# Kernel optimization log

Hardware: AMD Instinct MI355X
Metric: run time of the kernel (lower is better)

The kernel has to match this reference:

```python
import jax, jax.numpy as jnp
import numpy as np

B, S, D, H = 4, 1024, 1024, 16
DK = D // H
NEG = -1e9


def setup_inputs() -> dict:
    key = jax.random.key(0)
    ks = jax.random.split(key, 14)
    sc = 1.0 / np.sqrt(D)
    inp = {
        "query": jax.random.normal(ks[0], (B, S, D), jnp.float32),
        "key": jax.random.normal(ks[1], (B, S, D), jnp.float32),
        "value": jax.random.normal(ks[2], (B, S, D), jnp.float32),
        "mask": jax.random.randint(ks[3], (B, S, S), 0, 2, jnp.int32),
        "group_prob": jax.random.uniform(ks[4], (B, S, S), jnp.float32),
        "Wq": jax.random.normal(ks[5], (D, D), jnp.float32) * sc,
        "bq": jnp.zeros((D,), jnp.float32),
        "Wk": jax.random.normal(ks[6], (D, D), jnp.float32) * sc,
        "bk": jnp.zeros((D,), jnp.float32),
        "Wv": jax.random.normal(ks[7], (D, D), jnp.float32) * sc,
        "bv": jnp.zeros((D,), jnp.float32),
        "Wo": jax.random.normal(ks[8], (D, D), jnp.float32) * sc,
        "bo": jnp.zeros((D,), jnp.float32),
    }
    return inp


def reference(query, key, value, mask, group_prob, Wq, bq, Wk, bk, Wv, bv, Wo, bo):
    # QKV projections, split heads: [B,S,D] -> [B,H,S,DK]
    def proj(x, W, b):
        return (x @ W.T + b).reshape(B, S, H, DK).transpose(0, 2, 1, 3)

    q = proj(query, Wq, bq)
    k = proj(key, Wk, bk)
    v = proj(value, Wv, bv)

    scores = jnp.einsum("bhqd,bhkd->bhqk", q, k) / jnp.sqrt(jnp.float32(DK))

    # group_prob branch: allowed where mask OR diagonal is nonzero
    diag = jnp.eye(S, dtype=jnp.int32)
    allowed = (mask[:, None, :, :] | diag[None, None, :, :]) != 0  # [B,1,S,S]
    scores = jnp.where(allowed, scores, NEG)

    p_attn = jax.nn.softmax(scores, axis=-1)
    p_attn = p_attn * group_prob[:, None, :, :]  # post-softmax group reweighting

    x = jnp.einsum("bhqk,bhkd->bhqd", p_attn, v)
    x = x.transpose(0, 2, 1, 3).reshape(B, S, D)
    return x @ Wo.T + bo
```

## Files before the change

kernel.cpp:

```cpp
#include <hip/hip_runtime.h>
#include <hip/hip_bf16.h>


#define AS1q __attribute__((address_space(1)))
#define AS3q __attribute__((address_space(3)))

typedef __attribute__((ext_vector_type(8))) __bf16 bf16x8;
typedef __attribute__((ext_vector_type(4))) float f32x4;
typedef __attribute__((ext_vector_type(8))) unsigned short u16x8;

#define GSTR 40

__device__ __forceinline__ void gload_lds16(const void* g, void* l) {
  __builtin_amdgcn_global_load_lds((const AS1q void*)g, (AS3q void*)l, 16, 0, 0);
}
__device__ __forceinline__ bf16x8 lds_read8(const unsigned short* p) {
  bf16x8 r;
  __builtin_memcpy(&r, __builtin_assume_aligned(p, 16), 16);
  return r;
}
__device__ __forceinline__ void lds_write8(unsigned short* p, const void* v) {
  __builtin_memcpy(__builtin_assume_aligned(p, 16), v, 16);
}
__device__ __forceinline__ u16x8 cvt8h(const float4 a, const float4 b) {
  const float fv[8] = {a.x, a.y, a.z, a.w, b.x, b.y, b.z, b.w};
  union { u16x8 v; __bf16 e[8]; } hh;
#pragma unroll
  for (int i = 0; i < 8; ++i) hh.e[i] = (__bf16)fv[i];
  return hh.v;
}
__device__ __forceinline__ void cvt8hl(const float4 a, const float4 b, u16x8* hi, u16x8* lo) {
  const float fv[8] = {a.x, a.y, a.z, a.w, b.x, b.y, b.z, b.w};
  union { u16x8 v; __bf16 e[8]; } hh, ll;
#pragma unroll
  for (int i = 0; i < 8; ++i) {
    const __bf16 h = (__bf16)fv[i];
    hh.e[i] = h;
    ll.e[i] = (__bf16)(fv[i] - (float)h);
  }
  *hi = hh.v; *lo = ll.v;
}
__device__ __forceinline__ unsigned short bfbits(float f) {
  const __bf16 h = (__bf16)f;
  unsigned short u; __builtin_memcpy(&u, &h, 2); return u;
}

__global__ __launch_bounds__(256) void k_prep_g2(
    const int* __restrict__ Mask, const float* __restrict__ Gp, float* __restrict__ G2)
{
  const size_t f = (size_t)blockIdx.x * 256 + threadIdx.x;
  const size_t e = f << 2;
  const int k0 = (int)(e & 1023), q = (int)((e >> 10) & 1023);
  const int4 m4 = *(const int4*)(Mask + e);
  const float4 g4 = *(const float4*)(Gp + e);
  float4 r;
  r.x = (m4.x | (q == k0 + 0)) ? g4.x : -1.f;
  r.y = (m4.y | (q == k0 + 1)) ? g4.y : -1.f;
  r.z = (m4.z | (q == k0 + 2)) ? g4.z : -1.f;
  r.w = (m4.w | (q == k0 + 3)) ? g4.w : -1.f;
  *(float4*)(G2 + e) = r;
}

__global__ __launch_bounds__(256) void k_prep_w(
    const float* __restrict__ Wq, const float* __restrict__ Wk,
    const float* __restrict__ Wv,
    unsigned short* __restrict__ Qw, unsigned short* __restrict__ Kw,
    unsigned short* __restrict__ Vw)
{
  const int z = blockIdx.z;
  const size_t e = ((size_t)blockIdx.x * 256 + threadIdx.x) * 8;
  const float* S = (z == 0) ? Wq : (z == 1) ? Wk : Wv;
  unsigned short* D = (z == 0) ? Qw : (z == 1) ? Kw : Vw;
  const float4 a = *(const float4*)(S + e);
  const float4 b = *(const float4*)(S + e + 4);
  *(u16x8*)(D + e) = cvt8h(a, b);
}

__global__ __launch_bounds__(256) void k_gemm_qkv(
    const float* __restrict__ X0, const float* __restrict__ X1, const float* __restrict__ X2,
    const unsigned short* __restrict__ W0, const unsigned short* __restrict__ W1,
    const unsigned short* __restrict__ W2,
    const float* __restrict__ B0, const float* __restrict__ B1, const float* __restrict__ B2,
    unsigned short* __restrict__ O0, unsigned short* __restrict__ O1,
    unsigned short* __restrict__ O2)
{
  const int z = blockIdx.z;
  const float* X = (z == 0) ? X0 : (z == 1) ? X1 : X2;
  const unsigned short* W = (z == 0) ? W0 : (z == 1) ? W1 : W2;
  const float* Bi = (z == 0) ? B0 : (z == 1) ? B1 : B2;
  unsigned short* O = (z == 0) ? O0 : (z == 1) ? O1 : O2;

  const int bid = blockIdx.x;
  const int swz = (bid & 7) * 64 + (bid >> 3);
  const int n0 = (swz & 15) * 64, m0 = (swz >> 4) * 128;

  __shared__ alignas(16) unsigned short Ah[2][128 * GSTR];
  __shared__ alignas(16) unsigned short Bh[2][64 * GSTR];
  const int tid = threadIdx.x, l = tid & 63, w = tid >> 6;
  const int wr = w >> 1, wc = w & 1;

  f32x4 acc[4][2];
#pragma unroll
  for (int i = 0; i < 4; ++i)
#pragma unroll
    for (int j = 0; j < 2; ++j) acc[i][j] = (f32x4){0.f, 0.f, 0.f, 0.f};

  const int arow = tid >> 1, ac0 = (tid & 1) * 16;
  const int brow = tid >> 2, bc0 = (tid & 3) * 8;
  const float* xsrc = X + (size_t)(m0 + arow) * 1024 + ac0;
  const unsigned short* wsrc = W + (size_t)(n0 + brow) * 1024 + bc0;

  float4 fx[4];
  u16x8 bx;
#pragma unroll
  for (int i = 0; i < 4; ++i) fx[i] = *(const float4*)(xsrc + i * 4);
  bx = *(const u16x8*)(wsrc);
  {
    const u16x8 a0 = cvt8h(fx[0], fx[1]), a1 = cvt8h(fx[2], fx[3]);
    lds_write8(&Ah[0][arow * GSTR + ac0], &a0);
    lds_write8(&Ah[0][arow * GSTR + ac0 + 8], &a1);
    lds_write8(&Bh[0][brow * GSTR + bc0], &bx);
  }
#pragma unroll
  for (int i = 0; i < 4; ++i) fx[i] = *(const float4*)(xsrc + 32 + i * 4);
  bx = *(const u16x8*)(wsrc + 32);

  int buf = 0;
  for (int kt = 0; kt < 32; ++kt) {
    __syncthreads();
    if (kt < 31) {
      const u16x8 a0 = cvt8h(fx[0], fx[1]), a1 = cvt8h(fx[2], fx[3]);
      lds_write8(&Ah[buf ^ 1][arow * GSTR + ac0], &a0);
      lds_write8(&Ah[buf ^ 1][arow * GSTR + ac0 + 8], &a1);
      lds_write8(&Bh[buf ^ 1][brow * GSTR + bc0], &bx);
      if (kt < 30) {
        const float* nx = xsrc + (kt + 2) * 32;
#pragma unroll
        for (int i = 0; i < 4; ++i) fx[i] = *(const float4*)(nx + i * 4);
        bx = *(const u16x8*)(wsrc + (kt + 2) * 32);
      }
    }
    bf16x8 ah[4], bh[2];
#pragma unroll
    for (int mf = 0; mf < 4; ++mf) {
      const int r = wr * 64 + mf * 16 + (l & 15);
      ah[mf] = lds_read8(&Ah[buf][r * GSTR + (l >> 4) * 8]);
    }
#pragma unroll
    for (int nf = 0; nf < 2; ++nf) {
      const int r = wc * 32 + nf * 16 + (l & 15);
      bh[nf] = lds_read8(&Bh[buf][r * GSTR + (l >> 4) * 8]);
    }
#pragma unroll
    for (int mf = 0; mf < 4; ++mf)
#pragma unroll
      for (int nf = 0; nf < 2; ++nf)
        acc[mf][nf] = __builtin_amdgcn_mfma_f32_16x16x32_bf16(ah[mf], bh[nf], acc[mf][nf], 0, 0, 0);
    buf ^= 1;
  }

#pragma unroll
  for (int nf = 0; nf < 2; ++nf) {
    const int col = n0 + wc * 32 + nf * 16 + (l & 15);
    const float bias = Bi[col];
#pragma unroll
    for (int mf = 0; mf < 4; ++mf) {
      const int rbase = m0 + wr * 64 + mf * 16 + (l >> 4) * 4;
#pragma unroll
      for (int j = 0; j < 4; ++j)
        O[(size_t)(rbase + j) * 1024 + col] = bfbits(acc[mf][nf][j] + bias);
    }
  }
}

__global__ __launch_bounds__(256) void k_gemm_out(
    const unsigned short* __restrict__ X, const float* __restrict__ W,
    const float* __restrict__ Bi, float* __restrict__ Out)
{
  const int bid = blockIdx.x;
  const int swz = (bid & 7) * 128 + (bid >> 3);
  const int n0 = (swz & 15) * 64, m0 = (swz >> 4) * 64;

  __shared__ alignas(16) unsigned short Ah[64 * GSTR];
  __shared__ alignas(16) unsigned short Bh[64 * GSTR], Bl[64 * GSTR];
  const int tid = threadIdx.x, l = tid & 63, w = tid >> 6;
  const int wr = w >> 1, wc = w & 1;

  f32x4 acc[2][2];
#pragma unroll
  for (int i = 0; i < 2; ++i)
#pragma unroll
    for (int j = 0; j < 2; ++j) acc[i][j] = (f32x4){0.f, 0.f, 0.f, 0.f};

  const int srow = tid >> 2, sc0 = (tid & 3) * 8;
  const unsigned short* xsrc = X + (size_t)(m0 + srow) * 1024 + sc0;
  const float* wsrc = W + (size_t)(n0 + srow) * 1024 + sc0;

  u16x8 xcur = *(const u16x8*)xsrc;
  float4 fw[2];
#pragma unroll
  for (int i = 0; i < 2; ++i) fw[i] = *(const float4*)(wsrc + i * 4);

  for (int kt = 0; kt < 32; ++kt) {
    const u16x8 xstage = xcur;
    u16x8 wh1, wl1;
    cvt8hl(fw[0], fw[1], &wh1, &wl1);
    if (kt < 31) {
      xcur = *(const u16x8*)(xsrc + (kt + 1) * 32);
      const float* nw = wsrc + (kt + 1) * 32;
#pragma unroll
      for (int i = 0; i < 2; ++i) fw[i] = *(const float4*)(nw + i * 4);
    }
    __syncthreads();
    lds_write8(&Ah[srow * GSTR + sc0], &xstage);
    lds_write8(&Bh[srow * GSTR + sc0], &wh1);
    lds_write8(&Bl[srow * GSTR + sc0], &wl1);
    __syncthreads();

    bf16x8 ah[2], bh[2], bl[2];
#pragma unroll
    for (int mf = 0; mf < 2; ++mf) {
      const int r = wr * 32 + mf * 16 + (l & 15);
      ah[mf] = lds_read8(&Ah[r * GSTR + (l >> 4) * 8]);
    }
#pragma unroll
    for (int nf = 0; nf < 2; ++nf) {
      const int r = wc * 32 + nf * 16 + (l & 15);
      bh[nf] = lds_read8(&Bh[r * GSTR + (l >> 4) * 8]);
      bl[nf] = lds_read8(&Bl[r * GSTR + (l >> 4) * 8]);
    }
#pragma unroll
    for (int mf = 0; mf < 2; ++mf)
#pragma unroll
      for (int nf = 0; nf < 2; ++nf) {
        acc[mf][nf] = __builtin_amdgcn_mfma_f32_16x16x32_bf16(ah[mf], bh[nf], acc[mf][nf], 0, 0, 0);
        acc[mf][nf] = __builtin_amdgcn_mfma_f32_16x16x32_bf16(ah[mf], bl[nf], acc[mf][nf], 0, 0, 0);
      }
  }

#pragma unroll
  for (int nf = 0; nf < 2; ++nf) {
    const int col = n0 + wc * 32 + nf * 16 + (l & 15);
    const float bias = Bi[col];
#pragma unroll
    for (int mf = 0; mf < 2; ++mf) {
      const int rbase = m0 + wr * 32 + mf * 16 + (l >> 4) * 4;
#pragma unroll
      for (int j = 0; j < 4; ++j)
        Out[(size_t)(rbase + j) * 1024 + col] = acc[mf][nf][j] + bias;
    }
  }
}

__global__ __launch_bounds__(256) void k_attn(
    const unsigned short* Qh, const unsigned short* __restrict__ Kb,
    const unsigned short* __restrict__ Vb,
    const float* __restrict__ G2, unsigned short* Xo)
{
  const int i = blockIdx.x;
  const int xc = i & 7, kk_ = i >> 3;
  const int h = kk_ & 15, g = kk_ >> 4;
  const int qb = g * 8 + xc;
  const int qt = qb >> 2, b = qb & 3;

  __shared__ alignas(16) unsigned short Kh[2][64 * 64];
  __shared__ alignas(16) unsigned short Vh[64 * 64];
  __shared__ alignas(16) unsigned short Ph[64 * 64];
  const int tid = threadIdx.x, l = tid & 63, w = tid >> 6;

  const unsigned short* kb_ = Kb + (size_t)b * 1048576 + h * 64;
  const unsigned short* vb_ = Vb + (size_t)b * 1048576 + h * 64;

  bf16x8 aq[2];
  {
    const int qrow = qt * 64 + w * 16 + (l & 15);
    const unsigned short* qp_ = Qh + ((size_t)(b * 1024 + qrow)) * 1024 + h * 64;
    aq[0] = lds_read8(qp_ + (l >> 4) * 8);
    aq[1] = lds_read8(qp_ + 32 + (l >> 4) * 8);
  }

  f32x4 accO[4];
#pragma unroll
  for (int nf = 0; nf < 4; ++nf) accO[nf] = (f32x4){0.f, 0.f, 0.f, 0.f};
  float zacc[4] = {0.f, 0.f, 0.f, 0.f};

  const int qloc0 = w * 16 + (l >> 4) * 4;
  const int qg0 = qt * 64 + qloc0;
  const int mcol = l & 15;

  const float* grow[4];
#pragma unroll
  for (int j = 0; j < 4; ++j)
    grow[j] = G2 + (((size_t)(b * 1024 + qg0 + j)) << 10) + mcol;

  const int srcg8 = ((l & 7) ^ (l >> 3)) * 8;
  const int rowl = l >> 3;
  const int kb4 = (tid & 15) * 4, db4 = (tid >> 4) * 4;
  union U4 { unsigned int u[2]; unsigned short s[4]; };
  U4 vr[4];

#pragma unroll
  for (int I = 0; I < 2; ++I)
    gload_lds16(kb_ + (size_t)(I * 32 + w * 8 + rowl) * 1024 + srcg8,
                &Kh[0][I * 2048 + w * 512]);
#pragma unroll
  for (int ii = 0; ii < 4; ++ii)
    __builtin_memcpy(&vr[ii], vb_ + (size_t)(kb4 + ii) * 1024 + db4, 8);

  float gcur[4][4], gnext[4][4];
#pragma unroll
  for (int nf = 0; nf < 4; ++nf)
#pragma unroll
    for (int j = 0; j < 4; ++j) gcur[nf][j] = grow[j][nf * 16];

  int buf = 0;
  for (int kt = 0; kt < 16; ++kt) {
    __syncthreads();

#pragma unroll
    for (int ii = 0; ii < 4; ++ii) {
      const int d = db4 + ii;
      union { unsigned short s[4]; unsigned long long v; } pk;
#pragma unroll
      for (int u = 0; u < 4; ++u) pk.s[u] = vr[u].s[ii];
      const int c = kb4 ^ ((d & 7) << 3);
      __builtin_memcpy(__builtin_assume_aligned(&Vh[d * 64 + c], 8), &pk.v, 8);
    }
    __syncthreads();

    if (kt < 15) {
#pragma unroll
      for (int I = 0; I < 2; ++I)
        gload_lds16(kb_ + (size_t)((kt + 1) * 64 + I * 32 + w * 8 + rowl) * 1024 + srcg8,
                    &Kh[buf ^ 1][I * 2048 + w * 512]);
#pragma unroll
      for (int ii = 0; ii < 4; ++ii)
        __builtin_memcpy(&vr[ii], vb_ + (size_t)((kt + 1) * 64 + kb4 + ii) * 1024 + db4, 8);
#pragma unroll
      for (int nf = 0; nf < 4; ++nf)
#pragma unroll
        for (int j = 0; j < 4; ++j) gnext[nf][j] = grow[j][(kt + 1) * 64 + nf * 16];
    }

#pragma unroll
    for (int nf = 0; nf < 4; ++nf) {
      f32x4 sacc = (f32x4){0.f, 0.f, 0.f, 0.f};
      const int kr = nf * 16 + (l & 15);
#pragma unroll
      for (int ks = 0; ks < 2; ++ks) {
        const int c = (ks * 32 + (l >> 4) * 8) ^ ((kr & 7) << 3);
        sacc = __builtin_amdgcn_mfma_f32_16x16x32_bf16(aq[ks], lds_read8(&Kh[buf][kr * 64 + c]), sacc, 0, 0, 0);
      }
#pragma unroll
      for (int j = 0; j < 4; ++j) {
        const float g2 = gcur[nf][j];
        const float e = (g2 >= 0.f) ? exp2f(fmaf(sacc[j], 0.18033688f, -17.31234049f)) : 0.f;
        zacc[j] += e;
        const int qloc = qloc0 + j;
        Ph[qloc * 64 + ((nf * 16 + mcol) ^ ((qloc & 7) << 3))] = bfbits(e * g2);
      }
    }
    bf16x8 pah[2];
    {
      const int ar = w * 16 + (l & 15);
#pragma unroll
      for (int ks = 0; ks < 2; ++ks) {
        const int c = (ks * 32 + (l >> 4) * 8) ^ ((ar & 7) << 3);
        pah[ks] = lds_read8(&Ph[ar * 64 + c]);
      }
    }
#pragma unroll
    for (int nf = 0; nf < 4; ++nf) {
      const int dr = nf * 16 + (l & 15);
#pragma unroll
      for (int ks = 0; ks < 2; ++ks) {
        const int c = (ks * 32 + (l >> 4) * 8) ^ ((dr & 7) << 3);
        accO[nf] = __builtin_amdgcn_mfma_f32_16x16x32_bf16(pah[ks], lds_read8(&Vh[dr * 64 + c]), accO[nf], 0, 0, 0);
      }
    }
    buf ^= 1;
#pragma unroll
    for (int nf = 0; nf < 4; ++nf)
#pragma unroll
      for (int j = 0; j < 4; ++j) gcur[nf][j] = gnext[nf][j];
  }

#pragma unroll
  for (int j = 0; j < 4; ++j) {
#pragma unroll
    for (int off = 1; off < 16; off <<= 1) zacc[j] += __shfl_xor(zacc[j], off, 64);
  }
  float rz[4];
#pragma unroll
  for (int j = 0; j < 4; ++j) rz[j] = 1.f / zacc[j];

#pragma unroll
  for (int nf = 0; nf < 4; ++nf) {
    const int d = nf * 16 + (l & 15);
#pragma unroll
    for (int j = 0; j < 4; ++j) {
      const int qg = qg0 + j;
      Xo[((size_t)(b * 1024 + qg)) * 1024 + h * 64 + d] = bfbits(accO[nf][j] * rz[j]);
    }
  }
}

extern "C" void kernel_launch(void* const* d_in, const int* in_sizes, int n_in,
                              void* d_out, int out_size, void* d_ws, size_t ws_size,
                              hipStream_t stream) {
  const float* query = (const float*)d_in[0];
  const float* key_in = (const float*)d_in[1];
  const float* value = (const float*)d_in[2];
  const int* mask = (const int*)d_in[3];
  const float* gp = (const float*)d_in[4];
  const float* Wq = (const float*)d_in[5];
  const float* bq = (const float*)d_in[6];
  const float* Wk = (const float*)d_in[7];
  const float* bk = (const float*)d_in[8];
  const float* Wv = (const float*)d_in[9];
  const float* bv = (const float*)d_in[10];
  const float* Wo = (const float*)d_in[11];
  const float* bo = (const float*)d_in[12];
  float* out = (float*)d_out;

  unsigned short* kp = (unsigned short*)d_ws;
  unsigned short* vp = kp + 4194304;
  unsigned short* qp = vp + 4194304;
  unsigned short* xo = qp;
  float* g2 = (float*)(qp + 4194304);
  unsigned short* wq = (unsigned short*)(g2 + 4194304);
  unsigned short* wk = wq + 1048576;
  unsigned short* wv = wk + 1048576;

  hipLaunchKernelGGL(k_prep_g2, dim3(4096), dim3(256), 0, stream, mask, gp, g2);
  hipLaunchKernelGGL(k_prep_w, dim3(512, 1, 3), dim3(256), 0, stream,
                     Wq, Wk, Wv, wq, wk, wv);
  hipLaunchKernelGGL(k_gemm_qkv, dim3(512, 1, 3), dim3(256), 0, stream,
                     query, key_in, value, wq, wk, wv, bq, bk, bv, qp, kp, vp);
  hipLaunchKernelGGL(k_attn, dim3(1024), dim3(256), 0, stream,
                     qp, kp, vp, g2, xo);
  hipLaunchKernelGGL(k_gemm_out, dim3(1024), dim3(256), 0, stream,
                     xo, Wo, bo, out);
}
```

Measured before the change: 178.9 us.

## Pre-tile mask/group matrix into per-thread fragment order and double-buffer V

The prep kernel now writes the combined mask/group-probability matrix in a blocked layout matching each attention thread's MFMA fragment, so the attention kernel loads four contiguous float4s per tile instead of sixteen strided scalars. V is also double-buffered in LDS and prefetched two tiles ahead, which removes one barrier per iteration. The prep kernel's reads become scattered scalar loads, and LDS use grows by one 8KB buffer, which may lower occupancy.

Result: slower. 184.9 us (+3.3%).

```diff
diff --git a/kernel.cpp b/kernel.cpp
--- a/kernel.cpp
+++ b/kernel.cpp
@@ -46,19 +46,28 @@
 }
 
 __global__ __launch_bounds__(256) void k_prep_g2(
-    const int* __restrict__ Mask, const float* __restrict__ Gp, float* __restrict__ G2)
+    const int* __restrict__ Mask, const float* __restrict__ Gp, float* __restrict__ G2p)
 {
-  const size_t f = (size_t)blockIdx.x * 256 + threadIdx.x;
-  const size_t e = f << 2;
-  const int k0 = (int)(e & 1023), q = (int)((e >> 10) & 1023);
-  const int4 m4 = *(const int4*)(Mask + e);
-  const float4 g4 = *(const float4*)(Gp + e);
-  float4 r;
-  r.x = (m4.x | (q == k0 + 0)) ? g4.x : -1.f;
-  r.y = (m4.y | (q == k0 + 1)) ? g4.y : -1.f;
-  r.z = (m4.z | (q == k0 + 2)) ? g4.z : -1.f;
-  r.w = (m4.w | (q == k0 + 3)) ? g4.w : -1.f;
-  *(float4*)(G2 + e) = r;
+  const int bi = blockIdx.x;
+  const int kt = bi & 15, qt = (bi >> 4) & 15, b = bi >> 8;
+  const int t = threadIdx.x;
+  const int qbase = qt * 64 + ((t >> 6) << 4) + (((t >> 4) & 3) << 2);
+  const int kbase = kt * 64 + (t & 15);
+  float out[16];
+#pragma unroll
+  for (int nf = 0; nf < 4; ++nf) {
+    const int k = kbase + nf * 16;
+#pragma unroll
+    for (int j = 0; j < 4; ++j) {
+      const int q = qbase + j;
+      const size_t idx = (((size_t)(b * 1024 + q)) << 10) + k;
+      out[nf * 4 + j] = (Mask[idx] | (q == k)) ? Gp[idx] : -1.f;
+    }
+  }
+  float* dst = G2p + (size_t)bi * 4096 + t * 16;
+#pragma unroll
+  for (int i = 0; i < 4; ++i)
+    *(float4*)(dst + i * 4) = (float4){out[i * 4], out[i * 4 + 1], out[i * 4 + 2], out[i * 4 + 3]};
 }
 
 __global__ __launch_bounds__(256) void k_prep_w(
@@ -255,7 +264,7 @@
 __global__ __launch_bounds__(256) void k_attn(
     const unsigned short* Qh, const unsigned short* __restrict__ Kb,
     const unsigned short* __restrict__ Vb,
-    const float* __restrict__ G2, unsigned short* Xo)
+    const float* __restrict__ G2p, unsigned short* Xo)
 {
   const int i = blockIdx.x;
   const int xc = i & 7, kk_ = i >> 3;
@@ -264,12 +273,13 @@
   const int qt = qb >> 2, b = qb & 3;
 
   __shared__ alignas(16) unsigned short Kh[2][64 * 64];
-  __shared__ alignas(16) unsigned short Vh[64 * 64];
+  __shared__ alignas(16) unsigned short Vh[2][64 * 64];
   __shared__ alignas(16) unsigned short Ph[64 * 64];
   const int tid = threadIdx.x, l = tid & 63, w = tid >> 6;
 
   const unsigned short* kb_ = Kb + (size_t)b * 1048576 + h * 64;
   const unsigned short* vb_ = Vb + (size_t)b * 1048576 + h * 64;
+  const float* gbase = G2p + ((size_t)((b * 16 + qt) * 16)) * 4096 + tid * 16;
 
   bf16x8 aq[2];
   {
@@ -288,17 +298,13 @@
   const int qg0 = qt * 64 + qloc0;
   const int mcol = l & 15;
 
-  const float* grow[4];
-#pragma unroll
-  for (int j = 0; j < 4; ++j)
-    grow[j] = G2 + (((size_t)(b * 1024 + qg0 + j)) << 10) + mcol;
-
   const int srcg8 = ((l & 7) ^ (l >> 3)) * 8;
   const int rowl = l >> 3;
   const int kb4 = (tid & 15) * 4, db4 = (tid >> 4) * 4;
   union U4 { unsigned int u[2]; unsigned short s[4]; };
   U4 vr[4];
 
+  float4 gcur[4], gnext[4];
 #pragma unroll
   for (int I = 0; I < 2; ++I)
     gload_lds16(kb_ + (size_t)(I * 32 + w * 8 + rowl) * 1024 + srcg8,
@@ -306,40 +312,51 @@
 #pragma unroll
   for (int ii = 0; ii < 4; ++ii)
     __builtin_memcpy(&vr[ii], vb_ + (size_t)(kb4 + ii) * 1024 + db4, 8);
-
-  float gcur[4][4], gnext[4][4];
-#pragma unroll
-  for (int nf = 0; nf < 4; ++nf)
-#pragma unroll
-    for (int j = 0; j < 4; ++j) gcur[nf][j] = grow[j][nf * 16];
+#pragma unroll
+  for (int ii = 0; ii < 4; ++ii) gnext[ii] = *(const float4*)(gbase + ii * 4);
+  __syncthreads();
+#pragma unroll
+  for (int ii = 0; ii < 4; ++ii) {
+    const int d = db4 + ii;
+    union { unsigned short s[4]; unsigned long long v; } pk;
+#pragma unroll
+    for (int u = 0; u < 4; ++u) pk.s[u] = vr[u].s[ii];
+    const int c = kb4 ^ ((d & 7) << 3);
+    __builtin_memcpy(__builtin_assume_aligned(&Vh[0][d * 64 + c], 8), &pk.v, 8);
+  }
+#pragma unroll
+  for (int ii = 0; ii < 4; ++ii)
+    __builtin_memcpy(&vr[ii], vb_ + (size_t)(64 + kb4 + ii) * 1024 + db4, 8);
+  __syncthreads();
 
   int buf = 0;
   for (int kt = 0; kt < 16; ++kt) {
-    __syncthreads();
-
-#pragma unroll
-    for (int ii = 0; ii < 4; ++ii) {
-      const int d = db4 + ii;
-      union { unsigned short s[4]; unsigned long long v; } pk;
-#pragma unroll
-      for (int u = 0; u < 4; ++u) pk.s[u] = vr[u].s[ii];
-      const int c = kb4 ^ ((d & 7) << 3);
-      __builtin_memcpy(__builtin_assume_aligned(&Vh[d * 64 + c], 8), &pk.v, 8);
-    }
-    __syncthreads();
-
     if (kt < 15) {
+#pragma unroll
+      for (int ii = 0; ii < 4; ++ii) {
+        const int d = db4 + ii;
+        union { unsigned short s[4]; unsigned long long v; } pk;
+#pragma unroll
+        for (int u = 0; u < 4; ++u) pk.s[u] = vr[u].s[ii];
+        const int c = kb4 ^ ((d & 7) << 3);
+        __builtin_memcpy(__builtin_assume_aligned(&Vh[buf ^ 1][d * 64 + c], 8), &pk.v, 8);
+      }
 #pragma unroll
       for (int I = 0; I < 2; ++I)
         gload_lds16(kb_ + (size_t)((kt + 1) * 64 + I * 32 + w * 8 + rowl) * 1024 + srcg8,
                     &Kh[buf ^ 1][I * 2048 + w * 512]);
+      if (kt < 14) {
+#pragma unroll
+        for (int ii = 0; ii < 4; ++ii)
+          __builtin_memcpy(&vr[ii], vb_ + (size_t)((kt + 2) * 64 + kb4 + ii) * 1024 + db4, 8);
+      }
+    }
+#pragma unroll
+    for (int ii = 0; ii < 4; ++ii) gcur[ii] = gnext[ii];
+    if (kt < 15) {
 #pragma unroll
       for (int ii = 0; ii < 4; ++ii)
-        __builtin_memcpy(&vr[ii], vb_ + (size_t)((kt + 1) * 64 + kb4 + ii) * 1024 + db4, 8);
-#pragma unroll
-      for (int nf = 0; nf < 4; ++nf)
-#pragma unroll
-        for (int j = 0; j < 4; ++j) gnext[nf][j] = grow[j][(kt + 1) * 64 + nf * 16];
+        gnext[ii] = *(const float4*)(gbase + (size_t)(kt + 1) * 4096 + ii * 4);
     }
 
 #pragma unroll
@@ -351,9 +368,10 @@
         const int c = (ks * 32 + (l >> 4) * 8) ^ ((kr & 7) << 3);
         sacc = __builtin_amdgcn_mfma_f32_16x16x32_bf16(aq[ks], lds_read8(&Kh[buf][kr * 64 + c]), sacc, 0, 0, 0);
       }
+      const float gf[4] = {gcur[nf].x, gcur[nf].y, gcur[nf].z, gcur[nf].w};
 #pragma unroll
       for (int j = 0; j < 4; ++j) {
-        const float g2 = gcur[nf][j];
+        const float g2 = gf[j];
         const float e = (g2 >= 0.f) ? exp2f(fmaf(sacc[j], 0.18033688f, -17.31234049f)) : 0.f;
         zacc[j] += e;
         const int qloc = qloc0 + j;
@@ -375,14 +393,11 @@
 #pragma unroll
       for (int ks = 0; ks < 2; ++ks) {
         const int c = (ks * 32 + (l >> 4) * 8) ^ ((dr & 7) << 3);
-        accO[nf] = __builtin_amdgcn_mfma_f32_16x16x32_bf16(pah[ks], lds_read8(&Vh[dr * 64 + c]), accO[nf], 0, 0, 0);
-      }
-    }
+        accO[nf] = __builtin_amdgcn_mfma_f32_16x16x32_bf16(pah[ks], lds_read8(&Vh[buf][dr * 64 + c]), accO[nf], 0, 0, 0);
+      }
+    }
+    __syncthreads();
     buf ^= 1;
-#pragma unroll
-    for (int nf = 0; nf < 4; ++nf)
-#pragma unroll
-      for (int j = 0; j < 4; ++j) gcur[nf][j] = gnext[nf][j];
   }
 
 #pragma unroll
@@ -427,18 +442,18 @@
   unsigned short* vp = kp + 4194304;
   unsigned short* qp = vp + 4194304;
   unsigned short* xo = qp;
-  float* g2 = (float*)(qp + 4194304);
-  unsigned short* wq = (unsigned short*)(g2 + 4194304);
+  float* g2p = (float*)(qp + 4194304);
+  unsigned short* wq = (unsigned short*)(g2p + 4194304);
   unsigned short* wk = wq + 1048576;
   unsigned short* wv = wk + 1048576;
 
-  hipLaunchKernelGGL(k_prep_g2, dim3(4096), dim3(256), 0, stream, mask, gp, g2);
+  hipLaunchKernelGGL(k_prep_g2, dim3(1024), dim3(256), 0, stream, mask, gp, g2p);
   hipLaunchKernelGGL(k_prep_w, dim3(512, 1, 3), dim3(256), 0, stream,
                      Wq, Wk, Wv, wq, wk, wv);
   hipLaunchKernelGGL(k_gemm_qkv, dim3(512, 1, 3), dim3(256), 0, stream,
                      query, key_in, value, wq, wk, wv, bq, bk, bv, qp, kp, vp);
   hipLaunchKernelGGL(k_attn, dim3(1024), dim3(256), 0, stream,
-                     qp, kp, vp, g2, xo);
+                     qp, kp, vp, g2p, xo);
   hipLaunchKernelGGL(k_gemm_out, dim3(1024), dim3(256), 0, stream,
                      xo, Wo, bo, out);
 }
```

## Fuse mask/group-prob prep into QKV GEMM launch and double-buffer output GEMM

Applied to the files above, without the earlier changes.

Removes the separate k_prep_g2 kernel and runs its work as a fourth z-slice of the QKV GEMM grid, with each thread handling 16 elements. The grid grows to 1024 in x, and GEMM blocks past 512 exit early. This removes one launch and lets the bandwidth-bound mask prep overlap with the compute-bound GEMM blocks. Separately, the output-projection GEMM gets double-buffered LDS with one barrier per k-step instead of two, writing the next tile while the current one feeds the MFMAs. The cost is twice the LDS in k_gemm_out and 1536 idle blocks launched in the fused kernel.

Measured after the change: 180.7 us. Within noise of the previous version (+1.0%).

```diff
diff --git a/kernel.cpp b/kernel.cpp
--- a/kernel.cpp
+++ b/kernel.cpp
@@ -43,22 +43,6 @@
 __device__ __forceinline__ unsigned short bfbits(float f) {
   const __bf16 h = (__bf16)f;
   unsigned short u; __builtin_memcpy(&u, &h, 2); return u;
-}
-
-__global__ __launch_bounds__(256) void k_prep_g2(
-    const int* __restrict__ Mask, const float* __restrict__ Gp, float* __restrict__ G2)
-{
-  const size_t f = (size_t)blockIdx.x * 256 + threadIdx.x;
-  const size_t e = f << 2;
-  const int k0 = (int)(e & 1023), q = (int)((e >> 10) & 1023);
-  const int4 m4 = *(const int4*)(Mask + e);
-  const float4 g4 = *(const float4*)(Gp + e);
-  float4 r;
-  r.x = (m4.x | (q == k0 + 0)) ? g4.x : -1.f;
-  r.y = (m4.y | (q == k0 + 1)) ? g4.y : -1.f;
-  r.z = (m4.z | (q == k0 + 2)) ? g4.z : -1.f;
-  r.w = (m4.w | (q == k0 + 3)) ? g4.w : -1.f;
-  *(float4*)(G2 + e) = r;
 }
 
 __global__ __launch_bounds__(256) void k_prep_w(
@@ -76,15 +60,34 @@
   *(u16x8*)(D + e) = cvt8h(a, b);
 }
 
-__global__ __launch_bounds__(256) void k_gemm_qkv(
+__global__ __launch_bounds__(256) void k_qkv_g2(
     const float* __restrict__ X0, const float* __restrict__ X1, const float* __restrict__ X2,
     const unsigned short* __restrict__ W0, const unsigned short* __restrict__ W1,
     const unsigned short* __restrict__ W2,
     const float* __restrict__ B0, const float* __restrict__ B1, const float* __restrict__ B2,
     unsigned short* __restrict__ O0, unsigned short* __restrict__ O1,
-    unsigned short* __restrict__ O2)
+    unsigned short* __restrict__ O2,
+    const int* __restrict__ Mask, const float* __restrict__ Gp, float* __restrict__ G2)
 {
   const int z = blockIdx.z;
+  if (z == 3) {
+    const size_t e = ((size_t)blockIdx.x * 256 + threadIdx.x) * 16;
+    const int k0 = (int)(e & 1023), q = (int)((e >> 10) & 1023);
+#pragma unroll
+    for (int c = 0; c < 4; ++c) {
+      const int4 m4 = *(const int4*)(Mask + e + c * 4);
+      const float4 g4 = *(const float4*)(Gp + e + c * 4);
+      float4 r;
+      r.x = (m4.x | (q == k0 + c * 4 + 0)) ? g4.x : -1.f;
+      r.y = (m4.y | (q == k0 + c * 4 + 1)) ? g4.y : -1.f;
+      r.z = (m4.z | (q == k0 + c * 4 + 2)) ? g4.z : -1.f;
+      r.w = (m4.w | (q == k0 + c * 4 + 3)) ? g4.w : -1.f;
+      *(float4*)(G2 + e + c * 4) = r;
+    }
+    return;
+  }
+  if (blockIdx.x >= 512) return;
+
   const float* X = (z == 0) ? X0 : (z == 1) ? X1 : X2;
   const unsigned short* W = (z == 0) ? W0 : (z == 1) ? W1 : W2;
   const float* Bi = (z == 0) ? B0 : (z == 1) ? B1 : B2;
@@ -181,8 +184,8 @@
   const int swz = (bid & 7) * 128 + (bid >> 3);
   const int n0 = (swz & 15) * 64, m0 = (swz >> 4) * 64;
 
-  __shared__ alignas(16) unsigned short Ah[64 * GSTR];
-  __shared__ alignas(16) unsigned short Bh[64 * GSTR], Bl[64 * GSTR];
+  __shared__ alignas(16) unsigned short Ah[2][64 * GSTR];
+  __shared__ alignas(16) unsigned short Bh[2][64 * GSTR], Bl[2][64 * GSTR];
   const int tid = threadIdx.x, l = tid & 63, w = tid >> 6;
   const int wr = w >> 1, wc = w & 1;
 
@@ -200,34 +203,44 @@
   float4 fw[2];
 #pragma unroll
   for (int i = 0; i < 2; ++i) fw[i] = *(const float4*)(wsrc + i * 4);
-
-  for (int kt = 0; kt < 32; ++kt) {
-    const u16x8 xstage = xcur;
+  {
     u16x8 wh1, wl1;
     cvt8hl(fw[0], fw[1], &wh1, &wl1);
+    lds_write8(&Ah[0][srow * GSTR + sc0], &xcur);
+    lds_write8(&Bh[0][srow * GSTR + sc0], &wh1);
+    lds_write8(&Bl[0][srow * GSTR + sc0], &wl1);
+  }
+  xcur = *(const u16x8*)(xsrc + 32);
+#pragma unroll
+  for (int i = 0; i < 2; ++i) fw[i] = *(const float4*)(wsrc + 32 + i * 4);
+
+  int buf = 0;
+  for (int kt = 0; kt < 32; ++kt) {
+    __syncthreads();
     if (kt < 31) {
-      xcur = *(const u16x8*)(xsrc + (kt + 1) * 32);
-      const float* nw = wsrc + (kt + 1) * 32;
-#pragma unroll
-      for (int i = 0; i < 2; ++i) fw[i] = *(const float4*)(nw + i * 4);
-    }
-    __syncthreads();
-    lds_write8(&Ah[srow * GSTR + sc0], &xstage);
-    lds_write8(&Bh[srow * GSTR + sc0], &wh1);
-    lds_write8(&Bl[srow * GSTR + sc0], &wl1);
-    __syncthreads();
-
+      u16x8 wh1, wl1;
+      cvt8hl(fw[0], fw[1], &wh1, &wl1);
+      lds_write8(&Ah[buf ^ 1][srow * GSTR + sc0], &xcur);
+      lds_write8(&Bh[buf ^ 1][srow * GSTR + sc0], &wh1);
+      lds_write8(&Bl[buf ^ 1][srow * GSTR + sc0], &wl1);
+      if (kt < 30) {
+        xcur = *(const u16x8*)(xsrc + (kt + 2) * 32);
+        const float* nw = wsrc + (kt + 2) * 32;
+#pragma unroll
+        for (int i = 0; i < 2; ++i) fw[i] = *(const float4*)(nw + i * 4);
+      }
+    }
     bf16x8 ah[2], bh[2], bl[2];
 #pragma unroll
     for (int mf = 0; mf < 2; ++mf) {
       const int r = wr * 32 + mf * 16 + (l & 15);
-      ah[mf] = lds_read8(&Ah[r * GSTR + (l >> 4) * 8]);
+      ah[mf] = lds_read8(&Ah[buf][r * GSTR + (l >> 4) * 8]);
     }
 #pragma unroll
     for (int nf = 0; nf < 2; ++nf) {
       const int r = wc * 32 + nf * 16 + (l & 15);
-      bh[nf] = lds_read8(&Bh[r * GSTR + (l >> 4) * 8]);
-      bl[nf] = lds_read8(&Bl[r * GSTR + (l >> 4) * 8]);
+      bh[nf] = lds_read8(&Bh[buf][r * GSTR + (l >> 4) * 8]);
+      bl[nf] = lds_read8(&Bl[buf][r * GSTR + (l >> 4) * 8]);
     }
 #pragma unroll
     for (int mf = 0; mf < 2; ++mf)
@@ -236,6 +249,7 @@
         acc[mf][nf] = __builtin_amdgcn_mfma_f32_16x16x32_bf16(ah[mf], bh[nf], acc[mf][nf], 0, 0, 0);
         acc[mf][nf] = __builtin_amdgcn_mfma_f32_16x16x32_bf16(ah[mf], bl[nf], acc[mf][nf], 0, 0, 0);
       }
+    buf ^= 1;
   }
 
 #pragma unroll
@@ -432,11 +446,11 @@
   unsigned short* wk = wq + 1048576;
   unsigned short* wv = wk + 1048576;
 
-  hipLaunchKernelGGL(k_prep_g2, dim3(4096), dim3(256), 0, stream, mask, gp, g2);
   hipLaunchKernelGGL(k_prep_w, dim3(512, 1, 3), dim3(256), 0, stream,
                      Wq, Wk, Wv, wq, wk, wv);
-  hipLaunchKernelGGL(k_gemm_qkv, dim3(512, 1, 3), dim3(256), 0, stream,
-                     query, key_in, value, wq, wk, wv, bq, bk, bv, qp, kp, vp);
+  hipLaunchKernelGGL(k_qkv_g2, dim3(1024, 1, 4), dim3(256), 0, stream,
+                     query, key_in, value, wq, wk, wv, bq, bk, bv, qp, kp, vp,
+                     mask, gp, g2);
   hipLaunchKernelGGL(k_attn, dim3(1024), dim3(256), 0, stream,
                      qp, kp, vp, g2, xo);
   hipLaunchKernelGGL(k_gemm_out, dim3(1024), dim3(256), 0, stream,
```
